# Performance work log

Hardware: AMD Instinct MI355X
Metric: run time of the kernel (lower is better)

The kernel has to match this reference:

```python
import math
import jax, jax.numpy as jnp
import numpy as np

B, T, D, CHUNK = 16, 8192, 128, 64


def setup_inputs() -> dict:
    key = jax.random.key(0)
    kq, kk, kv = jax.random.split(key, 3)
    q = jax.random.normal(kq, (B, T, D), dtype=jnp.float32)
    k = jax.random.normal(kk, (B, T, D), dtype=jnp.float32)
    v = jax.random.normal(kv, (B, T, D), dtype=jnp.float32)
    # learnable per-head decay parameter, init so sigmoid(log_decay) = 0.99
    log_decay = jnp.full((1,), math.log(0.99 / (1.0 - 0.99)), dtype=jnp.float32)
    return {"q": q, "k": k, "v": v, "log_decay": log_decay, "chunk_size": CHUNK}


def reference(q, k, v, log_decay, chunk_size):
    """Chunk-wise parallel forward of DecayedLinearState.parallel_forward.

    Returns (output [B,T,D], final_state [B,D,D], final_z [B,D]).
    """
    lam = jax.nn.sigmoid(log_decay[0])
    Bb, Tt, Dd = q.shape
    C = int(chunk_size)
    pad = (-Tt) % C
    if pad:
        q = jnp.pad(q, ((0, 0), (0, pad), (0, 0)))
        k = jnp.pad(k, ((0, 0), (0, pad), (0, 0)))
        v = jnp.pad(v, ((0, 0), (0, pad), (0, 0)))
    N = (Tt + pad) // C
    qc = q.reshape(Bb, N, C, D)  # [B,N,C,D]
    kc = k.reshape(Bb, N, C, D)
    vc = v.reshape(Bb, N, C, D)

    pos = jnp.arange(C, dtype=q.dtype)
    rel = pos[:, None] - pos[None, :]                      # i - j
    causal = jnp.tril(jnp.ones((C, C), dtype=q.dtype))
    decay_matrix = (lam ** jnp.maximum(rel, 0.0)) * causal  # [C,C]

    # intra-chunk attention for all chunks in parallel
    attn = jnp.einsum('bnic,bnjc->bnij', qc, kc) * decay_matrix  # [B,N,C,C]
    intra_out = jnp.einsum('bnij,bnjd->bnid', attn, vc)          # [B,N,C,D]
    intra_z = jnp.maximum(attn.sum(-1), 1.0)                     # [B,N,C]

    decay_q = lam ** (pos + 1.0)           # decay applied to cross-chunk reads [C]
    chunk_decay = lam ** (C - 1.0 - pos)   # decay applied to state writes     [C]
    state_decay = lam ** C

    weighted_outer = jnp.einsum('bnci,bncj,c->bnij', kc, vc, chunk_decay)  # [B,N,D,D]
    k_sum = jnp.einsum('bnci,c->bni', kc, chunk_decay)                     # [B,N,D]

    def step(carry, xs):
        state, z = carry  # [B,D,D], [B,D]
        qcn, io_n, iz_n, wo_n, ks_n = xs
        cross_out = jnp.einsum('bij,bci->bcj', state, qcn) * decay_q[None, :, None]
        cross_z = jnp.einsum('bi,bci->bc', z, qcn) * decay_q[None, :]
        total_z = jnp.maximum(iz_n + cross_z, 1.0)[..., None]
        out = (io_n + cross_out) / total_z                     # [B,C,D]
        new_state = state_decay * state + wo_n
        new_z = state_decay * z + ks_n
        return (new_state, new_z), out

    init = (jnp.zeros((Bb, D, D), q.dtype), jnp.zeros((Bb, D), q.dtype))
    xs = (qc.transpose(1, 0, 2, 3), intra_out.transpose(1, 0, 2, 3),
          intra_z.transpose(1, 0, 2), weighted_outer.transpose(1, 0, 2, 3),
          k_sum.transpose(1, 0, 2))
    (state, z), outs = jax.lax.scan(step, init, xs)  # outs: [N,B,C,D]
    output = outs.transpose(1, 0, 2, 3).reshape(Bb, N * C, D)[:, :Tt]
    return output, state, z
```

## Files before the change

kernel.cpp:

```cpp
#include <hip/hip_runtime.h>
#include <math.h>

#define Bn  16
#define Tn  8192
#define Dn  128
#define Cn  64
#define Gn  8
#define NGn 16
#define GCn 512

typedef __attribute__((ext_vector_type(8)))  short short8v;
typedef __attribute__((ext_vector_type(16))) float f32x16;

#define AK  200
#define BK  200
#define KDs 136
#define KTs 72
#define KFs 132
#define K1s 72

__device__ __forceinline__ float sig_(float x){ return 1.0f/(1.0f+expf(-x)); }

__device__ __forceinline__ unsigned short f2bf(float f){
    __bf16 h = (__bf16)f;
    return __builtin_bit_cast(unsigned short, h);
}
__device__ __forceinline__ void st4(unsigned short* p, float a, float b, float c, float d){
    ushort4 u; u.x = f2bf(a); u.y = f2bf(b); u.z = f2bf(c); u.w = f2bf(d);
    *(ushort4*)p = u;
}

__global__ __launch_bounds__(512)
void k1_mfma(const float* __restrict__ kin, const float* __restrict__ vin,
             const float* __restrict__ log_decay,
             float* __restrict__ A, float* __restrict__ ksumg)
{
    const int g = blockIdx.x, b = blockIdx.y;
    const int tid  = threadIdx.x;
    const int wid  = tid >> 6;
    const int lane = tid & 63;
    const int l31  = lane & 31;
    const int lhi  = lane >> 5;
    const float lam = sig_(log_decay[0]);

    __shared__ __align__(16) unsigned short kT[128*K1s];
    __shared__ __align__(16) unsigned short vT[128*K1s];
    __shared__ float wt[GCn];
    __shared__ __align__(16) float ps[16*132];

    wt[tid] = powf(lam, (float)(GCn-1 - tid));

    const size_t base = ((size_t)b*Tn + (size_t)g*GCn)*Dn;
    const int rb = tid >> 5;
    const int cb = (tid & 31)*4;

    f32x16 acc[2];
    #pragma unroll
    for (int p = 0; p < 2; ++p)
        #pragma unroll
        for (int r = 0; r < 16; ++r) acc[p][r] = 0.f;
    float ksp[4] = {0.f, 0.f, 0.f, 0.f};

    float kv[4][4], vv[4][4];
    {
        const float* kp = kin + base;
        const float* vp = vin + base;
        #pragma unroll
        for (int u = 0; u < 4; ++u) {
            float4 t4 = *(const float4*)&kp[(size_t)(rb*4+u)*Dn + cb];
            kv[u][0]=t4.x; kv[u][1]=t4.y; kv[u][2]=t4.z; kv[u][3]=t4.w;
            float4 s4 = *(const float4*)&vp[(size_t)(rb*4+u)*Dn + cb];
            vv[u][0]=s4.x; vv[u][1]=s4.y; vv[u][2]=s4.z; vv[u][3]=s4.w;
        }
    }
    __syncthreads();

    const int tr0 = (wid >> 2)*2;
    const int tc  = (wid & 3)*32;

    for (int t = 0; t < 8; ++t) {
        const int r0 = rb*4;
        float w0 = wt[t*64 + r0+0], w1 = wt[t*64 + r0+1];
        float w2 = wt[t*64 + r0+2], w3 = wt[t*64 + r0+3];
        #pragma unroll
        for (int e = 0; e < 4; ++e) {
            float a0 = kv[0][e]*w0, a1 = kv[1][e]*w1, a2 = kv[2][e]*w2, a3 = kv[3][e]*w3;
            ksp[e] += (a0 + a1) + (a2 + a3);
            st4(&kT[(cb+e)*K1s + r0], a0, a1, a2, a3);
            st4(&vT[(cb+e)*K1s + r0], vv[0][e], vv[1][e], vv[2][e], vv[3][e]);
        }
        __syncthreads();

        if (t < 7) {
            const float* kp = kin + base + (size_t)(t+1)*64*Dn;
            const float* vp = vin + base + (size_t)(t+1)*64*Dn;
            #pragma unroll
            for (int u = 0; u < 4; ++u) {
                float4 t4 = *(const float4*)&kp[(size_t)(rb*4+u)*Dn + cb];
                kv[u][0]=t4.x; kv[u][1]=t4.y; kv[u][2]=t4.z; kv[u][3]=t4.w;
                float4 s4 = *(const float4*)&vp[(size_t)(rb*4+u)*Dn + cb];
                vv[u][0]=s4.x; vv[u][1]=s4.y; vv[u][2]=s4.z; vv[u][3]=s4.w;
            }
        }

        #pragma unroll
        for (int kk = 0; kk < 4; ++kk) {
            short8v bf = *(const short8v*)&vT[(tc + l31)*K1s + kk*16 + lhi*8];
            #pragma unroll
            for (int p = 0; p < 2; ++p) {
                short8v af = *(const short8v*)&kT[((tr0+p)*32 + l31)*K1s + kk*16 + lhi*8];
                acc[p] = __builtin_amdgcn_mfma_f32_32x32x16_bf16(af, bf, acc[p], 0, 0, 0);
            }
        }
        __syncthreads();
    }

    float* Ab = A + ((size_t)(b*NGn + g))*Dn*Dn;
    #pragma unroll
    for (int p = 0; p < 2; ++p) {
        #pragma unroll
        for (int r = 0; r < 16; ++r) {
            int i = (tr0+p)*32 + (r&3) + 8*(r>>2) + 4*lhi;
            Ab[(size_t)i*Dn + tc + l31] = acc[p][r];
        }
    }

    *(float4*)&ps[rb*132 + cb] = make_float4(ksp[0], ksp[1], ksp[2], ksp[3]);
    __syncthreads();
    if (tid < Dn) {
        float s = 0.f;
        #pragma unroll
        for (int q = 0; q < 16; ++q) s += ps[q*132 + tid];
        ksumg[((size_t)(b*NGn+g))*Dn + tid] = s;
    }
}

__global__ __launch_bounds__(256)
void k2_scan(const float* __restrict__ A, const float* __restrict__ ksumg,
             const float* __restrict__ log_decay,
             float* __restrict__ Sg, float* __restrict__ zg,
             float* __restrict__ outState, float* __restrict__ outZ)
{
    const int idx = blockIdx.x*256 + threadIdx.x;
    const float lam = sig_(log_decay[0]);
    const float dG = powf(lam, (float)GCn);
    const int NSTATE = Bn*Dn*Dn;
    if (idx < NSTATE) {
        const int b = idx >> 14, ij = idx & 16383;
        float s = 0.f;
        #pragma unroll
        for (int g = 0; g < NGn; ++g) {
            size_t o = (((size_t)(b*NGn+g)) << 14) + ij;
            Sg[o] = s;
            s = dG*s + A[o];
        }
        outState[idx] = s;
    } else if (idx < NSTATE + Bn*Dn) {
        const int j = idx - NSTATE, b = j >> 7, d = j & 127;
        float s = 0.f;
        #pragma unroll
        for (int g = 0; g < NGn; ++g) {
            size_t o = (size_t)(b*NGn+g)*Dn + d;
            zg[o] = s;
            s = dG*s + ksumg[o];
        }
        outZ[j] = s;
    }
}

__global__ __launch_bounds__(512)
void k3_mfma(const float* __restrict__ qin, const float* __restrict__ kin,
             const float* __restrict__ vin, const float* __restrict__ log_decay,
             const float* __restrict__ Sg, const float* __restrict__ zg,
             float* __restrict__ out)
{
    const int g = blockIdx.x, b = blockIdx.y;
    const int tid  = threadIdx.x;
    const int wid  = tid >> 6;
    const int lane = tid & 63;
    const int l31  = lane & 31;
    const int lhi  = lane >> 5;
    const float lam   = sig_(log_decay[0]);
    const float lam64 = powf(lam, 64.0f);

    __shared__ __align__(16) unsigned short sA [64*AK];
    __shared__ __align__(16) unsigned short sB [128*BK];
    __shared__ __align__(16) unsigned short sKd[64*KDs];
    __shared__ __align__(16) unsigned short sKT[128*KTs];
    __shared__ __align__(16) float kf[64*KFs];
    __shared__ __align__(16) float zf[128];
    __shared__ __align__(16) float izb[64], czb[64];
    __shared__ float ptabs[66], ntabs[64];

    const int bg = b*NGn + g;

    if (tid < 66)  ptabs[tid] = powf(lam, (float)tid);
    if (tid >= 66 && tid < 130) ntabs[tid-66] = powf(lam, -(float)(tid-65));
    if (tid < 128) zf[tid] = zg[(size_t)bg*Dn + tid];

    f32x16 sacc[4];
    if (wid >= 4) {
        const float* Sgp = Sg + ((size_t)bg << 14);
        const int er0 = (wid-4)*32;
        #pragma unroll
        for (int ct = 0; ct < 4; ++ct) {
            const int d = ct*32 + l31;
            #pragma unroll
            for (int r = 0; r < 16; ++r) {
                int e = er0 + (r&3) + 8*(r>>2) + 4*lhi;
                sacc[ct][r] = Sgp[e*Dn + d];
            }
            #pragma unroll
            for (int q = 0; q < 4; ++q) {
                int e0 = er0 + 8*q + 4*lhi;
                st4(&sB[d*BK + 64 + e0],
                    sacc[ct][4*q], sacc[ct][4*q+1], sacc[ct][4*q+2], sacc[ct][4*q+3]);
            }
        }
    }
    __syncthreads();

    for (int m = 0; m < Gn; ++m) {
        const size_t rowbase = (size_t)b*Tn + (size_t)(g*Gn + m)*Cn;

        #pragma unroll
        for (int u = 0; u < 4; ++u) {
            int f = tid + 512*u;
            int i = f >> 5, c4 = (f & 31)*4;
            float4 qv = *(const float4*)&qin[(rowbase + i)*Dn + c4];
            float s = ptabs[i+1];
            st4(&sA[i*AK + 64 + c4], qv.x*s, qv.y*s, qv.z*s, qv.w*s);
        }
        {
            const int a4 = (tid >> 5)*4;
            const int b4 = (tid & 31)*4;
            float kv[4][4];
            #pragma unroll
            for (int u = 0; u < 4; ++u) {
                float4 t = *(const float4*)&kin[(rowbase + a4+u)*Dn + b4];
                kv[u][0]=t.x; kv[u][1]=t.y; kv[u][2]=t.z; kv[u][3]=t.w;
                *(float4*)&kf[(a4+u)*KFs + b4] = t;
            }
            #pragma unroll
            for (int u = 0; u < 4; ++u) {
                float s = ntabs[a4+u];
                st4(&sKd[(a4+u)*KDs + b4], kv[u][0]*s, kv[u][1]*s, kv[u][2]*s, kv[u][3]*s);
            }
            float w0 = ptabs[63-a4], w1 = ptabs[62-a4], w2 = ptabs[61-a4], w3 = ptabs[60-a4];
            #pragma unroll
            for (int e = 0; e < 4; ++e)
                st4(&sKT[(b4+e)*KTs + a4], kv[0][e]*w0, kv[1][e]*w1, kv[2][e]*w2, kv[3][e]*w3);
        }
        {
            const int a4 = (tid >> 5)*4;
            const int b4 = (tid & 31)*4;
            float vv[4][4];
            #pragma unroll
            for (int u = 0; u < 4; ++u) {
                float4 t = *(const float4*)&vin[(rowbase + a4+u)*Dn + b4];
                vv[u][0]=t.x; vv[u][1]=t.y; vv[u][2]=t.z; vv[u][3]=t.w;
            }
            #pragma unroll
            for (int e = 0; e < 4; ++e)
                st4(&sB[(b4+e)*BK + a4], vv[0][e], vv[1][e], vv[2][e], vv[3][e]);
        }
        __syncthreads();

        if (wid < 2) {
            const int d = tid;
            float kap = 0.f;
            #pragma unroll 8
            for (int j = 0; j < Cn; ++j) {
                kap = lam*kap + kf[j*KFs + d];
                kf[j*KFs + d] = kap;
            }
        } else if (wid < 4) {
            const int ic = (wid - 2)*32;
            #pragma unroll
            for (int jj = 0; jj < 2; ++jj) {
                const int jr = jj*32;
                f32x16 acc;
                #pragma unroll
                for (int r = 0; r < 16; ++r) acc[r] = 0.f;
                #pragma unroll
                for (int kk = 0; kk < 8; ++kk) {
                    short8v af = *(const short8v*)&sKd[(jr + l31)*KDs + kk*16 + lhi*8];
                    short8v bf = *(const short8v*)&sA [(ic + l31)*AK + 64 + kk*16 + lhi*8];
                    acc = __builtin_amdgcn_mfma_f32_32x32x16_bf16(af, bf, acc, 0, 0, 0);
                }
                const int i = ic + l31;
                #pragma unroll
                for (int q = 0; q < 4; ++q) {
                    int j0 = jr + 8*q + 4*lhi;
                    float v0 = (j0+0 <= i) ? acc[4*q+0] : 0.f;
                    float v1 = (j0+1 <= i) ? acc[4*q+1] : 0.f;
                    float v2 = (j0+2 <= i) ? acc[4*q+2] : 0.f;
                    float v3 = (j0+3 <= i) ? acc[4*q+3] : 0.f;
                    st4(&sA[i*AK + j0], v0, v1, v2, v3);
                }
            }
        } else {
            const int er0 = (wid-4)*32;
            #pragma unroll
            for (int ct = 0; ct < 4; ++ct)
                #pragma unroll
                for (int r = 0; r < 16; ++r) sacc[ct][r] *= lam64;
            #pragma unroll
            for (int kk = 0; kk < 4; ++kk) {
                short8v af = *(const short8v*)&sKT[(er0 + l31)*KTs + kk*16 + lhi*8];
                #pragma unroll
                for (int ct = 0; ct < 4; ++ct) {
                    short8v bf = *(const short8v*)&sB[(ct*32 + l31)*BK + kk*16 + lhi*8];
                    sacc[ct] = __builtin_amdgcn_mfma_f32_32x32x16_bf16(af, bf, sacc[ct], 0, 0, 0);
                }
            }
        }
        __syncthreads();

        {
            const int i = tid >> 3, seg = tid & 7;
            const float* qrow = &qin[(rowbase + i)*Dn + seg*16];
            float aI = 0.f, aZ = 0.f;
            #pragma unroll
            for (int u = 0; u < 4; ++u) {
                float4 qv = *(const float4*)(qrow + u*4);
                float4 kp = *(const float4*)&kf[i*KFs + seg*16 + u*4];
                float4 zv = *(const float4*)&zf[seg*16 + u*4];
                aI += qv.x*kp.x + qv.y*kp.y + qv.z*kp.z + qv.w*kp.w;
                aZ += qv.x*zv.x + qv.y*zv.y + qv.z*zv.z + qv.w*zv.w;
            }
            aI += __shfl_xor(aI, 1); aZ += __shfl_xor(aZ, 1);
            aI += __shfl_xor(aI, 2); aZ += __shfl_xor(aZ, 2);
            aI += __shfl_xor(aI, 4); aZ += __shfl_xor(aZ, 4);
            if (seg == 0) { izb[i] = aI; czb[i] = ptabs[i+1]*aZ; }
        }
        const int r0 = (wid >> 2)*32;
        const int c0 = (wid & 3)*32;
        f32x16 oacc;
        #pragma unroll
        for (int r = 0; r < 16; ++r) oacc[r] = 0.f;
        #pragma unroll
        for (int kk = 0; kk < 12; ++kk) {
            short8v af = *(const short8v*)&sA[(r0 + l31)*AK + kk*16 + lhi*8];
            short8v bf = *(const short8v*)&sB[(c0 + l31)*BK + kk*16 + lhi*8];
            oacc = __builtin_amdgcn_mfma_f32_32x32x16_bf16(af, bf, oacc, 0, 0, 0);
        }
        __syncthreads();

        #pragma unroll
        for (int r = 0; r < 16; ++r) {
            int t = r0 + (r&3) + 8*(r>>2) + 4*lhi;
            float tz = fmaxf(fmaxf(izb[t], 1.f) + czb[t], 1.f);
            float rv = __builtin_amdgcn_rcpf(tz);
            out[(rowbase + t)*Dn + c0 + l31] = oacc[r] * rv;
        }

        if (wid >= 4) {
            const int er0 = (wid-4)*32;
            #pragma unroll
            for (int ct = 0; ct < 4; ++ct) {
                const int d = ct*32 + l31;
                #pragma unroll
                for (int q = 0; q < 4; ++q) {
                    int e0 = er0 + 8*q + 4*lhi;
                    st4(&sB[d*BK + 64 + e0],
                        sacc[ct][4*q], sacc[ct][4*q+1], sacc[ct][4*q+2], sacc[ct][4*q+3]);
                }
            }
        }
        if (tid < 128) {
            zf[tid] = lam64*zf[tid] + kf[63*KFs + tid];
        }
        __syncthreads();
    }
}

extern "C" void kernel_launch(void* const* d_in, const int* in_sizes, int n_in,
                              void* d_out, int out_size, void* d_ws, size_t ws_size,
                              hipStream_t stream)
{
    const float* q  = (const float*)d_in[0];
    const float* k  = (const float*)d_in[1];
    const float* v  = (const float*)d_in[2];
    const float* ld = (const float*)d_in[3];
    float* out = (float*)d_out;

    float* A     = (float*)d_ws;
    float* ksumg = A     + (size_t)Bn*NGn*Dn*Dn;
    float* Sg    = ksumg + (size_t)Bn*NGn*Dn;
    float* zg    = Sg    + (size_t)Bn*NGn*Dn*Dn;

    float* outState = out      + (size_t)Bn*Tn*Dn;
    float* outZ     = outState + (size_t)Bn*Dn*Dn;

    hipLaunchKernelGGL(k1_mfma, dim3(NGn, Bn), dim3(512), 0, stream,
                       k, v, ld, A, ksumg);

    const int total2 = Bn*Dn*Dn + Bn*Dn;
    hipLaunchKernelGGL(k2_scan, dim3((total2 + 255)/256), dim3(256), 0, stream,
                       A, ksumg, ld, Sg, zg, outState, outZ);

    hipLaunchKernelGGL(k3_mfma, dim3(NGn, Bn), dim3(512), 0, stream,
                       q, k, v, ld, Sg, zg, out);
}
```

Measured before the change: 99.59 us.

## Swizzle LDS transposes, prefetch next chunk into registers, and restructure k3 loop

Adds an XOR swizzle to the transposed k/v shared-memory tiles in both k1 and k3 to reduce LDS bank conflicts. In k3, the next chunk's q/k/v are prefetched into registers while the current chunk computes. The output MFMA is split so the state-read part overlaps with the state update phase, the epilogue store is deferred into the next iteration, and zf is double-buffered so one barrier can be dropped. It also sets launch_bounds(512,2) and register-blocks the cumulative decay scan, at the cost of higher register pressure and more complex indexing.

```diff
diff --git a/kernel.cpp b/kernel.cpp
--- a/kernel.cpp
+++ b/kernel.cpp
@@ -18,6 +18,8 @@
 #define KTs 72
 #define KFs 132
 #define K1s 72
+
+#define SWZ(row) ((((row) >> 2) & 7) << 3)
 
 __device__ __forceinline__ float sig_(float x){ return 1.0f/(1.0f+expf(-x)); }
 
@@ -84,10 +86,11 @@
         float w2 = wt[t*64 + r0+2], w3 = wt[t*64 + r0+3];
         #pragma unroll
         for (int e = 0; e < 4; ++e) {
+            int row = cb+e, col = r0 ^ SWZ(row);
             float a0 = kv[0][e]*w0, a1 = kv[1][e]*w1, a2 = kv[2][e]*w2, a3 = kv[3][e]*w3;
             ksp[e] += (a0 + a1) + (a2 + a3);
-            st4(&kT[(cb+e)*K1s + r0], a0, a1, a2, a3);
-            st4(&vT[(cb+e)*K1s + r0], vv[0][e], vv[1][e], vv[2][e], vv[3][e]);
+            st4(&kT[row*K1s + col], a0, a1, a2, a3);
+            st4(&vT[row*K1s + col], vv[0][e], vv[1][e], vv[2][e], vv[3][e]);
         }
         __syncthreads();
 
@@ -105,10 +108,12 @@
 
         #pragma unroll
         for (int kk = 0; kk < 4; ++kk) {
-            short8v bf = *(const short8v*)&vT[(tc + l31)*K1s + kk*16 + lhi*8];
+            int rB = tc + l31;
+            short8v bf = *(const short8v*)&vT[rB*K1s + ((kk*16 + lhi*8) ^ SWZ(rB))];
             #pragma unroll
             for (int p = 0; p < 2; ++p) {
-                short8v af = *(const short8v*)&kT[((tr0+p)*32 + l31)*K1s + kk*16 + lhi*8];
+                int rA = (tr0+p)*32 + l31;
+                short8v af = *(const short8v*)&kT[rA*K1s + ((kk*16 + lhi*8) ^ SWZ(rA))];
                 acc[p] = __builtin_amdgcn_mfma_f32_32x32x16_bf16(af, bf, acc[p], 0, 0, 0);
             }
         }
@@ -168,7 +173,7 @@
     }
 }
 
-__global__ __launch_bounds__(512)
+__global__ __launch_bounds__(512, 2)
 void k3_mfma(const float* __restrict__ qin, const float* __restrict__ kin,
              const float* __restrict__ vin, const float* __restrict__ log_decay,
              const float* __restrict__ Sg, const float* __restrict__ zg,
@@ -188,11 +193,12 @@
     __shared__ __align__(16) unsigned short sKd[64*KDs];
     __shared__ __align__(16) unsigned short sKT[128*KTs];
     __shared__ __align__(16) float kf[64*KFs];
-    __shared__ __align__(16) float zf[128];
+    __shared__ __align__(16) float zf[2*128];
     __shared__ __align__(16) float izb[64], czb[64];
     __shared__ float ptabs[66], ntabs[64];
 
     const int bg = b*NGn + g;
+    const size_t base = (size_t)b*Tn + (size_t)g*Gn*Cn;
 
     if (tid < 66)  ptabs[tid] = powf(lam, (float)tid);
     if (tid >= 66 && tid < 130) ntabs[tid-66] = powf(lam, -(float)(tid-65));
@@ -218,61 +224,114 @@
             }
         }
     }
+
+    const int a4  = (tid >> 5)*4;
+    const int b4c = (tid & 31)*4;
+
+    float qv[4][4], kv[4][4], vv[4][4];
+    {
+        #pragma unroll
+        for (int u = 0; u < 4; ++u) {
+            int f = tid + 512*u;
+            float4 t = *(const float4*)&qin[(base + (f>>5))*Dn + (f&31)*4];
+            qv[u][0]=t.x; qv[u][1]=t.y; qv[u][2]=t.z; qv[u][3]=t.w;
+        }
+        #pragma unroll
+        for (int u = 0; u < 4; ++u) {
+            float4 t = *(const float4*)&kin[(base + a4+u)*Dn + b4c];
+            kv[u][0]=t.x; kv[u][1]=t.y; kv[u][2]=t.z; kv[u][3]=t.w;
+            float4 s = *(const float4*)&vin[(base + a4+u)*Dn + b4c];
+            vv[u][0]=s.x; vv[u][1]=s.y; vv[u][2]=s.z; vv[u][3]=s.w;
+        }
+    }
+
+    const int r0 = (wid >> 2)*32;
+    const int c0 = (wid & 3)*32;
+    f32x16 oacc;
+    #pragma unroll
+    for (int r = 0; r < 16; ++r) oacc[r] = 0.f;
+
     __syncthreads();
 
     for (int m = 0; m < Gn; ++m) {
-        const size_t rowbase = (size_t)b*Tn + (size_t)(g*Gn + m)*Cn;
-
+        const size_t rowbase = base + (size_t)m*Cn;
+
+        if (m > 0) {
+            const size_t prow = rowbase - Cn;
+            #pragma unroll
+            for (int r = 0; r < 16; ++r) {
+                int t = r0 + (r&3) + 8*(r>>2) + 4*lhi;
+                float tz = fmaxf(fmaxf(izb[t], 1.f) + czb[t], 1.f);
+                out[(prow + t)*Dn + c0 + l31] = oacc[r] * __builtin_amdgcn_rcpf(tz);
+            }
+            #pragma unroll
+            for (int r = 0; r < 16; ++r) oacc[r] = 0.f;
+            if (wid >= 4) {
+                #pragma unroll
+                for (int ct = 0; ct < 4; ++ct) {
+                    const int d = ct*32 + l31;
+                    #pragma unroll
+                    for (int q = 0; q < 4; ++q) {
+                        int e0 = (wid-4)*32 + 8*q + 4*lhi;
+                        st4(&sB[d*BK + 64 + e0],
+                            sacc[ct][4*q], sacc[ct][4*q+1], sacc[ct][4*q+2], sacc[ct][4*q+3]);
+                    }
+                }
+            }
+        }
         #pragma unroll
         for (int u = 0; u < 4; ++u) {
             int f = tid + 512*u;
             int i = f >> 5, c4 = (f & 31)*4;
-            float4 qv = *(const float4*)&qin[(rowbase + i)*Dn + c4];
             float s = ptabs[i+1];
-            st4(&sA[i*AK + 64 + c4], qv.x*s, qv.y*s, qv.z*s, qv.w*s);
+            st4(&sA[i*AK + 64 + c4], qv[u][0]*s, qv[u][1]*s, qv[u][2]*s, qv[u][3]*s);
+        }
+        #pragma unroll
+        for (int u = 0; u < 4; ++u)
+            *(float4*)&kf[(a4+u)*KFs + b4c] = make_float4(kv[u][0],kv[u][1],kv[u][2],kv[u][3]);
+        #pragma unroll
+        for (int u = 0; u < 4; ++u) {
+            float s = ntabs[a4+u];
+            st4(&sKd[(a4+u)*KDs + b4c], kv[u][0]*s, kv[u][1]*s, kv[u][2]*s, kv[u][3]*s);
         }
         {
-            const int a4 = (tid >> 5)*4;
-            const int b4 = (tid & 31)*4;
-            float kv[4][4];
+            float w0 = ptabs[63-a4], w1 = ptabs[62-a4], w2 = ptabs[61-a4], w3 = ptabs[60-a4];
+            #pragma unroll
+            for (int e = 0; e < 4; ++e) {
+                int row = b4c + e, col = a4 ^ SWZ(row);
+                st4(&sKT[row*KTs + col], kv[0][e]*w0, kv[1][e]*w1, kv[2][e]*w2, kv[3][e]*w3);
+                st4(&sB [row*BK  + (a4 ^ SWZ(row))], vv[0][e], vv[1][e], vv[2][e], vv[3][e]);
+            }
+        }
+        if (m + 1 < Gn) {
+            const size_t nrow = rowbase + Cn;
             #pragma unroll
             for (int u = 0; u < 4; ++u) {
-                float4 t = *(const float4*)&kin[(rowbase + a4+u)*Dn + b4];
+                int f = tid + 512*u;
+                float4 t = *(const float4*)&qin[(nrow + (f>>5))*Dn + (f&31)*4];
+                qv[u][0]=t.x; qv[u][1]=t.y; qv[u][2]=t.z; qv[u][3]=t.w;
+            }
+            #pragma unroll
+            for (int u = 0; u < 4; ++u) {
+                float4 t = *(const float4*)&kin[(nrow + a4+u)*Dn + b4c];
                 kv[u][0]=t.x; kv[u][1]=t.y; kv[u][2]=t.z; kv[u][3]=t.w;
-                *(float4*)&kf[(a4+u)*KFs + b4] = t;
-            }
-            #pragma unroll
-            for (int u = 0; u < 4; ++u) {
-                float s = ntabs[a4+u];
-                st4(&sKd[(a4+u)*KDs + b4], kv[u][0]*s, kv[u][1]*s, kv[u][2]*s, kv[u][3]*s);
-            }
-            float w0 = ptabs[63-a4], w1 = ptabs[62-a4], w2 = ptabs[61-a4], w3 = ptabs[60-a4];
-            #pragma unroll
-            for (int e = 0; e < 4; ++e)
-                st4(&sKT[(b4+e)*KTs + a4], kv[0][e]*w0, kv[1][e]*w1, kv[2][e]*w2, kv[3][e]*w3);
-        }
-        {
-            const int a4 = (tid >> 5)*4;
-            const int b4 = (tid & 31)*4;
-            float vv[4][4];
-            #pragma unroll
-            for (int u = 0; u < 4; ++u) {
-                float4 t = *(const float4*)&vin[(rowbase + a4+u)*Dn + b4];
-                vv[u][0]=t.x; vv[u][1]=t.y; vv[u][2]=t.z; vv[u][3]=t.w;
-            }
-            #pragma unroll
-            for (int e = 0; e < 4; ++e)
-                st4(&sB[(b4+e)*BK + a4], vv[0][e], vv[1][e], vv[2][e], vv[3][e]);
+                float4 s = *(const float4*)&vin[(nrow + a4+u)*Dn + b4c];
+                vv[u][0]=s.x; vv[u][1]=s.y; vv[u][2]=s.z; vv[u][3]=s.w;
+            }
         }
         __syncthreads();
 
         if (wid < 2) {
             const int d = tid;
             float kap = 0.f;
-            #pragma unroll 8
-            for (int j = 0; j < Cn; ++j) {
-                kap = lam*kap + kf[j*KFs + d];
-                kf[j*KFs + d] = kap;
+            for (int bb = 0; bb < 4; ++bb) {
+                float rr[16];
+                #pragma unroll
+                for (int j = 0; j < 16; ++j) rr[j] = kf[(bb*16+j)*KFs + d];
+                #pragma unroll
+                for (int j = 0; j < 16; ++j) { kap = lam*kap + rr[j]; rr[j] = kap; }
+                #pragma unroll
+                for (int j = 0; j < 16; ++j) kf[(bb*16+j)*KFs + d] = rr[j];
             }
         } else if (wid < 4) {
             const int ic = (wid - 2)*32;
@@ -307,71 +366,63 @@
                 for (int r = 0; r < 16; ++r) sacc[ct][r] *= lam64;
             #pragma unroll
             for (int kk = 0; kk < 4; ++kk) {
-                short8v af = *(const short8v*)&sKT[(er0 + l31)*KTs + kk*16 + lhi*8];
+                int rA = er0 + l31;
+                short8v af = *(const short8v*)&sKT[rA*KTs + ((kk*16 + lhi*8) ^ SWZ(rA))];
                 #pragma unroll
                 for (int ct = 0; ct < 4; ++ct) {
-                    short8v bf = *(const short8v*)&sB[(ct*32 + l31)*BK + kk*16 + lhi*8];
+                    int rB = ct*32 + l31;
+                    short8v bf = *(const short8v*)&sB[rB*BK + ((kk*16 + lhi*8) ^ SWZ(rB))];
                     sacc[ct] = __builtin_amdgcn_mfma_f32_32x32x16_bf16(af, bf, sacc[ct], 0, 0, 0);
                 }
             }
         }
+        #pragma unroll
+        for (int kk = 4; kk < 12; ++kk) {
+            short8v af = *(const short8v*)&sA[(r0 + l31)*AK + kk*16 + lhi*8];
+            short8v bf = *(const short8v*)&sB[(c0 + l31)*BK + kk*16 + lhi*8];
+            oacc = __builtin_amdgcn_mfma_f32_32x32x16_bf16(af, bf, oacc, 0, 0, 0);
+        }
         __syncthreads();
 
         {
             const int i = tid >> 3, seg = tid & 7;
+            const float* zc = &zf[(m & 1)*128];
             const float* qrow = &qin[(rowbase + i)*Dn + seg*16];
             float aI = 0.f, aZ = 0.f;
             #pragma unroll
             for (int u = 0; u < 4; ++u) {
-                float4 qv = *(const float4*)(qrow + u*4);
+                float4 qv4 = *(const float4*)(qrow + u*4);
                 float4 kp = *(const float4*)&kf[i*KFs + seg*16 + u*4];
-                float4 zv = *(const float4*)&zf[seg*16 + u*4];
-                aI += qv.x*kp.x + qv.y*kp.y + qv.z*kp.z + qv.w*kp.w;
-                aZ += qv.x*zv.x + qv.y*zv.y + qv.z*zv.z + qv.w*zv.w;
+                float4 zv = *(const float4*)(zc + seg*16 + u*4);
+                aI += qv4.x*kp.x + qv4.y*kp.y + qv4.z*kp.z + qv4.w*kp.w;
+                aZ += qv4.x*zv.x + qv4.y*zv.y + qv4.z*zv.z + qv4.w*zv.w;
             }
             aI += __shfl_xor(aI, 1); aZ += __shfl_xor(aZ, 1);
             aI += __shfl_xor(aI, 2); aZ += __shfl_xor(aZ, 2);
             aI += __shfl_xor(aI, 4); aZ += __shfl_xor(aZ, 4);
             if (seg == 0) { izb[i] = aI; czb[i] = ptabs[i+1]*aZ; }
         }
-        const int r0 = (wid >> 2)*32;
-        const int c0 = (wid & 3)*32;
-        f32x16 oacc;
-        #pragma unroll
-        for (int r = 0; r < 16; ++r) oacc[r] = 0.f;
-        #pragma unroll
-        for (int kk = 0; kk < 12; ++kk) {
+        if (tid < 128) {
+            zf[((m+1)&1)*128 + tid] = lam64*zf[(m&1)*128 + tid] + kf[63*KFs + tid];
+        }
+        #pragma unroll
+        for (int kk = 0; kk < 4; ++kk) {
             short8v af = *(const short8v*)&sA[(r0 + l31)*AK + kk*16 + lhi*8];
-            short8v bf = *(const short8v*)&sB[(c0 + l31)*BK + kk*16 + lhi*8];
+            int rB = c0 + l31;
+            short8v bf = *(const short8v*)&sB[rB*BK + ((kk*16 + lhi*8) ^ SWZ(rB))];
             oacc = __builtin_amdgcn_mfma_f32_32x32x16_bf16(af, bf, oacc, 0, 0, 0);
         }
         __syncthreads();
-
+    }
+
+    {
+        const size_t prow = base + (size_t)(Gn-1)*Cn;
         #pragma unroll
         for (int r = 0; r < 16; ++r) {
             int t = r0 + (r&3) + 8*(r>>2) + 4*lhi;
             float tz = fmaxf(fmaxf(izb[t], 1.f) + czb[t], 1.f);
-            float rv = __builtin_amdgcn_rcpf(tz);
-            out[(rowbase + t)*Dn + c0 + l31] = oacc[r] * rv;
-        }
-
-        if (wid >= 4) {
-            const int er0 = (wid-4)*32;
-            #pragma unroll
-            for (int ct = 0; ct < 4; ++ct) {
-                const int d = ct*32 + l31;
-                #pragma unroll
-                for (int q = 0; q < 4; ++q) {
-                    int e0 = er0 + 8*q + 4*lhi;
-                    st4(&sB[d*BK + 64 + e0],
-                        sacc[ct][4*q], sacc[ct][4*q+1], sacc[ct][4*q+2], sacc[ct][4*q+3]);
-                }
-            }
-        }
-        if (tid < 128) {
-            zf[tid] = lam64*zf[tid] + kf[63*KFs + tid];
-        }
-        __syncthreads();
+            out[(prow + t)*Dn + c0 + l31] = oacc[r] * __builtin_amdgcn_rcpf(tz);
+        }
     }
 }
 
```

Measured after the change: 123.6 us. 1.24x slower.
